# Performance work log

Hardware: AMD Instinct MI355X
Metric: run time of the kernel (lower is better)

## Reference

```python
import jax, jax.numpy as jnp
import numpy as np

E = 50000      # entity_total
R = 100        # relation_total
DIM = 128      # config.dim
M = 10         # max_context_num
M1 = M + 1
T = 2 * R + 2  # entity_gcn_weight rows (2R+1) + appended zero row
B = 1024


def setup_inputs() -> dict:
    key = jax.random.key(0)
    ks = jax.random.split(key, 40)
    f = jnp.float32
    stdv = 1.0 / np.sqrt(DIM)
    inp = {}
    inp['entity_emb'] = jax.random.normal(ks[0], (E, DIM), f) * 0.05
    inp['relation_emb'] = jax.random.normal(ks[1], (R, DIM), f) * 0.05
    ec = jax.random.normal(ks[2], (E + 1, DIM), f) * 0.05
    inp['entity_context'] = ec.at[E].set(0.0)   # padding_idx row = 0
    rc = jax.random.normal(ks[3], (R + 1, DIM), f) * 0.05
    inp['relation_context'] = rc.at[R].set(0.0)
    inp['entity_gcn_weight'] = jax.random.uniform(ks[4], (2 * R + 1, DIM, DIM), f, -stdv, stdv)
    inp['relation_gcn_weight'] = jax.random.uniform(ks[5], (DIM, DIM), f, -stdv, stdv)
    inp['gate_entity'] = jax.random.uniform(ks[6], (DIM,), f)
    inp['gate_relation'] = jax.random.uniform(ks[7], (DIM,), f)
    inp['v_ent'] = jax.random.uniform(ks[8], (DIM,), f)
    inp['v_rel'] = jax.random.uniform(ks[9], (DIM,), f)
    inp['pos_h'] = jax.random.randint(ks[10], (B,), 0, E)
    inp['pos_r'] = jax.random.randint(ks[11], (B,), 0, R)
    inp['pos_t'] = jax.random.randint(ks[12], (B,), 0, E)
    inp['neg_h'] = jax.random.randint(ks[13], (B,), 0, E)
    inp['neg_r'] = jax.random.randint(ks[14], (B,), 0, R)
    inp['neg_t'] = jax.random.randint(ks[15], (B,), 0, E)
    inp['ph_adj'] = jax.random.randint(ks[16], (B, M), 0, E + 1)
    inp['pt_adj'] = jax.random.randint(ks[17], (B, M), 0, E + 1)
    inp['nh_adj'] = jax.random.randint(ks[18], (B, M), 0, E + 1)
    inp['nt_adj'] = jax.random.randint(ks[19], (B, M), 0, E + 1)
    inp['pr_adj'] = jax.random.randint(ks[20], (B, M, 2), 0, R + 1)
    inp['nr_adj'] = jax.random.randint(ks[21], (B, M, 2), 0, R + 1)
    inp['ph_R'] = jax.random.randint(ks[22], (B, M1, M1), 0, T)
    inp['pt_R'] = jax.random.randint(ks[23], (B, M1, M1), 0, T)
    inp['nh_R'] = jax.random.randint(ks[24], (B, M1, M1), 0, T)
    inp['nt_R'] = jax.random.randint(ks[25], (B, M1, M1), 0, T)
    inp['ph_nn'] = jax.random.randint(ks[26], (B,), 0, M)
    inp['pt_nn'] = jax.random.randint(ks[27], (B,), 0, M)
    inp['nh_nn'] = jax.random.randint(ks[28], (B,), 0, M)
    inp['nt_nn'] = jax.random.randint(ks[29], (B,), 0, M)
    inp['ph_D'] = jax.random.uniform(ks[30], (B, M1, M1), f)
    inp['pt_D'] = jax.random.uniform(ks[31], (B, M1, M1), f)
    inp['nh_D'] = jax.random.uniform(ks[32], (B, M1, M1), f)
    inp['nt_D'] = jax.random.uniform(ks[33], (B, M1, M1), f)
    inp['pr_A'] = jax.random.normal(ks[34], (B, M1, M1), f)
    inp['nr_A'] = jax.random.normal(ks[35], (B, M1, M1), f)
    return inp


def reference(entity_emb, relation_emb, entity_context, relation_context,
              entity_gcn_weight, relation_gcn_weight, gate_entity, gate_relation,
              v_ent, v_rel,
              pos_h, pos_r, pos_t, neg_h, neg_r, neg_t,
              ph_adj, pt_adj, nh_adj, nt_adj, pr_adj, nr_adj,
              ph_R, pt_R, nh_R, nt_R, ph_nn, pt_nn, nh_nn, nt_nn,
              ph_D, pt_D, nh_D, nt_D, pr_A, nr_A):
    # weight table with trailing zero row (padding relation type T-1)
    Wfull = jnp.concatenate(
        [entity_gcn_weight, jnp.zeros((1, DIM, DIM), entity_gcn_weight.dtype)], axis=0)

    def ent_ctx(vec, adj_idx):
        # center vector + M gathered context vectors -> [B, M1, d]
        return jnp.concatenate([vec[:, None, :], entity_context[adj_idx]], axis=1)

    def rel_ctx(vec, adj_idx):
        # relation context comes in (head,tail) pairs, summed over the 2
        a = relation_context[adj_idx].sum(axis=2)  # [B, M, d]
        return jnp.concatenate([vec[:, None, :], a], axis=1)

    def rgcn(Rt, Dm, nn_, H):
        # vectorized R-GCN: out[b,j] = relu(sum_k D[b,j,k] * H[b,j] @ W[Rt[b,j,k]])
        # restricted to the dynamic (n+1)x(n+1) block via masking.
        j = jnp.arange(M1)
        valid = j[None, :] <= nn_[:, None]                 # [B, M1]
        pair = valid[:, :, None] & valid[:, None, :]       # [B, M1, M1]
        Rm = jnp.where(pair, Rt, T - 1)                    # pad -> zero weight
        Dd = jnp.where(pair, Dm, jnp.zeros((), Dm.dtype))
        # segment-reduce D over relation types: C[b,j,t] = sum_{k: Rm=t} D[b,j,k]
        C = (jax.nn.one_hot(Rm, T, dtype=H.dtype) * Dd[..., None]).sum(axis=2)  # [B,M1,T]
        S = jnp.einsum('bjt,tde->bjde', C, Wfull)          # [B, M1, d, d]
        out = jax.nn.relu(jnp.einsum('bjd,bjde->bje', H, S))
        return jnp.where(valid[..., None], out, jnp.zeros((), out.dtype))

    def gcn_rel(A, H):
        return jax.nn.relu(jnp.einsum('bij,bjd,de->bie', A, H, relation_gcn_weight))

    def subgraph(o, adj, v):
        # attention over context rows, then weighted sum
        tmp = jax.nn.relu(adj * o[:, None, :])             # [B, M1, d]
        alpha = jax.nn.softmax(tmp @ v, axis=1)            # [B, M1]
        return jnp.sum(alpha[..., None] * adj, axis=1)     # [B, d]

    p_h = entity_emb[pos_h]; p_t = entity_emb[pos_t]; p_r = relation_emb[pos_r]
    n_h = entity_emb[neg_h]; n_t = entity_emb[neg_t]; n_r = relation_emb[neg_r]

    ph_v = rgcn(ph_R, ph_D, ph_nn, ent_ctx(p_h, ph_adj))
    pt_v = rgcn(pt_R, pt_D, pt_nn, ent_ctx(p_t, pt_adj))
    nh_v = rgcn(nh_R, nh_D, nh_nn, ent_ctx(n_h, nh_adj))
    nt_v = rgcn(nt_R, nt_D, nt_nn, ent_ctx(n_t, nt_adj))
    pr_v = gcn_rel(pr_A, rel_ctx(p_r, pr_adj))
    nr_v = gcn_rel(nr_A, rel_ctx(n_r, nr_adj))

    ph_sg = subgraph(p_h, ph_v, v_ent); pt_sg = subgraph(p_t, pt_v, v_ent)
    nh_sg = subgraph(n_h, nh_v, v_ent); nt_sg = subgraph(n_t, nt_v, v_ent)
    pr_sg = subgraph(p_r, pr_v, v_rel); nr_sg = subgraph(n_r, nr_v, v_rel)

    ge = jax.nn.sigmoid(gate_entity)
    gr = jax.nn.sigmoid(gate_relation)
    ph_o = ge * p_h + (1 - ge) * ph_sg
    pt_o = ge * p_t + (1 - ge) * pt_sg
    nh_o = ge * n_h + (1 - ge) * nh_sg
    nt_o = ge * n_t + (1 - ge) * nt_sg
    pr_o = gr * p_r + (1 - gr) * pr_sg
    nr_o = gr * n_r + (1 - gr) * nr_sg

    p_score = jnp.linalg.norm(ph_o + pr_o - pt_o, ord=2, axis=1)
    n_score = jnp.linalg.norm(nh_o + nr_o - nt_o, ord=2, axis=1)
    return (p_score, n_score)
```

## Files before the change

### kernel.cpp

```cpp
#include <hip/hip_runtime.h>
#include <math.h>

#define B_   1024
#define M_   10
#define M1_  11
#define DIM_ 128
#define NW_  201
#define NQUAD_ (4*B_*M1_*M1_)
#define IPB_  64
#define SLOTS_ 2048
#define SCATB_ 121
#define WTILES_ ((NW_+1)*16)
#define HROWS_ (4*B_*M1_)
#define HROWB_ (HROWS_/16)
#define GEMMB_ (NW_*32)

typedef __attribute__((ext_vector_type(8))) short bf16x8;
typedef __attribute__((ext_vector_type(4))) float f32x4;

struct GatherPtrs {
    const int* center[4];
    const int* adj[4];
    const int* nn[4];
    const int* Rt[4];
    const float* Dm[4];
};

struct RelPtrs {
    const int* center[2];
    const int* adj2[2];
    const float* A[2];
};

__device__ __forceinline__ unsigned short f2bf(float f) {
    union { float f; unsigned u; } v; v.f = f;
    const unsigned r = v.u + 0x7FFFu + ((v.u >> 16) & 1u);
    return (unsigned short)(r >> 16);
}

template <int N>
__device__ __forceinline__ void block_reduce_bcast(float (&p)[N], float (*sred)[N],
                                                   int e, float (&sc)[N])
{
    #pragma unroll
    for (int off = 32; off; off >>= 1)
        #pragma unroll
        for (int i = 0; i < N; ++i) p[i] += __shfl_xor(p[i], off, 64);
    __syncthreads();
    if ((e & 63) == 0) {
        #pragma unroll
        for (int i = 0; i < N; ++i) sred[e >> 6][i] = p[i];
    }
    __syncthreads();
    #pragma unroll
    for (int i = 0; i < N; ++i) sc[i] = sred[0][i] + sred[1][i];
}

__device__ __forceinline__ float attn_pool(const float (&vm)[M1_], float o, float ve,
                                           float (*sred)[M1_], int e)
{
    float p[M1_];
    #pragma unroll
    for (int j = 0; j < M1_; ++j) p[j] = fmaxf(vm[j] * o, 0.f) * ve;
    float sc[M1_];
    block_reduce_bcast<M1_>(p, sred, e, sc);
    float mx = sc[0];
    #pragma unroll
    for (int j = 1; j < M1_; ++j) mx = fmaxf(mx, sc[j]);
    float s = 0.f, ex[M1_];
    #pragma unroll
    for (int j = 0; j < M1_; ++j) { ex[j] = expf(sc[j] - mx); s += ex[j]; }
    const float inv = 1.f / s;
    float sg = 0.f;
    #pragma unroll
    for (int j = 0; j < M1_; ++j) sg += ex[j] * inv * vm[j];
    return sg;
}

__global__ __launch_bounds__(256)
void prep_kernel(GatherPtrs gp,
                 const float* __restrict__ W, const float* __restrict__ Wr,
                 const float* __restrict__ ent_emb,
                 const float* __restrict__ ent_ctx,
                 unsigned short* __restrict__ WT,
                 unsigned short* __restrict__ Hd,
                 int* __restrict__ cursor, int* __restrict__ items)
{
    __shared__ int lh[NW_];
    __shared__ int lbase[NW_];
    __shared__ float tile[32][33];
    const int tid = threadIdx.x;
    const int bid = blockIdx.x;

    if (bid < SCATB_) {
        if (tid < NW_) lh[tid] = 0;
        __syncthreads();
        int rr[16], rk[16], pk[16];
        #pragma unroll
        for (int s = 0; s < 16; ++s) {
            const int idx = bid * 4096 + s * 256 + tid;
            const int c = idx / (B_ * M1_ * M1_);
            const int rem = idx % (B_ * M1_ * M1_);
            const int b = rem / (M1_ * M1_);
            const int jk = rem % (M1_ * M1_);
            const int j = jk / M1_, k = jk % M1_;
            const int n = gp.nn[c][b];
            rr[s] = -1;
            if (j <= n && k <= n) {
                const int r = gp.Rt[c][rem];
                if (r < NW_) {
                    rr[s] = r;
                    rk[s] = atomicAdd(&lh[r], 1);
                    pk[s] = (c << 18) | (b << 8) | (j << 4) | k;
                }
            }
        }
        __syncthreads();
        if (tid < NW_) lbase[tid] = lh[tid] ? atomicAdd(&cursor[tid], lh[tid]) : 0;
        __syncthreads();
        #pragma unroll
        for (int s = 0; s < 16; ++s)
            if (rr[s] >= 0) {
                const int slot = lbase[rr[s]] + rk[s];
                if (slot < SLOTS_) items[rr[s] * SLOTS_ + slot] = pk[s];
            }
    } else if (bid < SCATB_ + WTILES_) {
        const int tl = bid - SCATB_;
        const int t = tl >> 4, sub = tl & 15;
        const int bd = (sub >> 2) * 32, be = (sub & 3) * 32;
        const float* Ws = (t < NW_) ? (W + (size_t)t * DIM_ * DIM_) : Wr;
        unsigned short* Wd = WT + (size_t)t * DIM_ * DIM_;
        const int tx = tid & 31, ty = tid >> 5;
        #pragma unroll
        for (int r = 0; r < 32; r += 8)
            tile[r + ty][tx] = Ws[(bd + r + ty) * DIM_ + be + tx];
        __syncthreads();
        #pragma unroll
        for (int r = 0; r < 32; r += 8)
            Wd[(be + r + ty) * DIM_ + bd + tx] = f2bf(tile[tx][r + ty]);
    } else {
        const int rid = (bid - SCATB_ - WTILES_) * 16 + (tid >> 4);
        const int part = tid & 15;
        const int c = rid / (B_ * M1_);
        const int rem = rid % (B_ * M1_);
        const int b = rem / M1_, j = rem % M1_;
        const float* srow = (j == 0)
            ? ent_emb + (size_t)gp.center[c][b] * DIM_
            : ent_ctx + (size_t)gp.adj[c][b * M_ + (j - 1)] * DIM_;
        const float4* s4 = (const float4*)srow + part * 2;
        const float4 v0 = s4[0], v1 = s4[1];
        uint4 pkd;
        pkd.x = (unsigned)f2bf(v0.x) | ((unsigned)f2bf(v0.y) << 16);
        pkd.y = (unsigned)f2bf(v0.z) | ((unsigned)f2bf(v0.w) << 16);
        pkd.z = (unsigned)f2bf(v1.x) | ((unsigned)f2bf(v1.y) << 16);
        pkd.w = (unsigned)f2bf(v1.z) | ((unsigned)f2bf(v1.w) << 16);
        *reinterpret_cast<uint4*>(Hd + (size_t)rid * DIM_ + part * 8) = pkd;
    }
}

template <int MODE>
__global__ __launch_bounds__(256)
void rgcn_gemm(GatherPtrs gp,
               const float* __restrict__ ent_emb,
               const float* __restrict__ ent_ctx,
               const unsigned short* __restrict__ WT,
               const unsigned short* __restrict__ Hd,
               const int* __restrict__ items,
               const int* __restrict__ cursor,
               _Float16* __restrict__ partial,
               float* __restrict__ vent)
{
    __shared__ unsigned short sH[IPB_ * DIM_];
    __shared__ int sQ[IPB_];
    __shared__ float sD[IPB_];

    const int bid = blockIdx.x;
    const int t = bid >> 5, ch = bid & 31;
    const int cnt = min(cursor[t], SLOTS_);
    if (ch * IPB_ >= cnt) return;
    const int istart = ch * IPB_;
    const int nItems = min(IPB_, cnt - istart);
    const int tid = threadIdx.x;
    const int* ibase = items + t * SLOTS_;

    #pragma unroll
    for (int it4 = 0; it4 < 4; ++it4) {
        const int m = it4 * 256 + tid;
        const int it = m >> 4, chd = m & 15;
        uint4 pkd;
        if (it < nItems) {
            const int p = ibase[istart + it];
            const int c = p >> 18, b = (p >> 8) & 1023, j = (p >> 4) & 15, k = p & 15;
            const int row = (c * B_ + b) * M1_ + j;
            if (chd == 0) {
                sQ[it] = row * M1_ + k;
                sD[it] = gp.Dm[c][(b * M1_ + j) * M1_ + k];
            }
            if (MODE == 1) {
                pkd = *reinterpret_cast<const uint4*>(Hd + (size_t)row * DIM_ + chd * 8);
            } else {
                const float* srow = (j == 0)
                    ? ent_emb + (size_t)gp.center[c][b] * DIM_
                    : ent_ctx + (size_t)gp.adj[c][b * M_ + (j - 1)] * DIM_;
                const float4* s4 = (const float4*)srow + chd * 2;
                const float4 v0 = s4[0], v1 = s4[1];
                pkd.x = (unsigned)f2bf(v0.x) | ((unsigned)f2bf(v0.y) << 16);
                pkd.y = (unsigned)f2bf(v0.z) | ((unsigned)f2bf(v0.w) << 16);
                pkd.z = (unsigned)f2bf(v1.x) | ((unsigned)f2bf(v1.y) << 16);
                pkd.w = (unsigned)f2bf(v1.z) | ((unsigned)f2bf(v1.w) << 16);
            }
        } else {
            if (chd == 0) { sQ[it] = -1; sD[it] = 0.f; }
            pkd.x = pkd.y = pkd.z = pkd.w = 0u;
        }
        const int so = it * 256 + ((chd * 16) ^ ((it & 7) << 4));
        *reinterpret_cast<uint4*>(reinterpret_cast<char*>(sH) + so) = pkd;
    }
    __syncthreads();

    const int w = tid >> 6, l = tid & 63;
    const int lr = l & 15, lk = l >> 4;
    const unsigned short* Wp = WT + (size_t)t * DIM_ * DIM_;
    const f32x4 z = {0.f, 0.f, 0.f, 0.f};
    f32x4 acc[4][2];
    #pragma unroll
    for (int mi = 0; mi < 4; ++mi) { acc[mi][0] = z; acc[mi][1] = z; }

    #pragma unroll
    for (int kb = 0; kb < 4; ++kb) {
        const int o = kb * 64 + lk * 16;
        bf16x8 af[4], bfr[2];
        #pragma unroll
        for (int ni = 0; ni < 2; ++ni) {
            const int row = (2 * w + ni) * 16 + lr;
            bfr[ni] = *reinterpret_cast<const bf16x8*>(Wp + (size_t)row * DIM_ + kb * 32 + lk * 8);
        }
        #pragma unroll
        for (int mi = 0; mi < 4; ++mi) {
            const int row = mi * 16 + lr;
            af[mi] = *reinterpret_cast<const bf16x8*>(
                reinterpret_cast<const char*>(sH) + row * 256 + (o ^ ((row & 7) << 4)));
        }
        #pragma unroll
        for (int mi = 0; mi < 4; ++mi)
            #pragma unroll
            for (int ni = 0; ni < 2; ++ni)
                acc[mi][ni] = __builtin_amdgcn_mfma_f32_16x16x32_bf16(
                    af[mi], bfr[ni], acc[mi][ni], 0, 0, 0);
    }

    #pragma unroll
    for (int mi = 0; mi < 4; ++mi) {
        #pragma unroll
        for (int jj = 0; jj < 4; ++jj) {
            const int it = mi * 16 + lk * 4 + jj;
            const int q = sQ[it];
            if (q >= 0) {
                const float d = sD[it];
                #pragma unroll
                for (int ni = 0; ni < 2; ++ni) {
                    const int col = (2 * w + ni) * 16 + lr;
                    const float val = acc[mi][ni][jj] * d;
                    if (MODE <= 1) {
                        partial[(size_t)q * DIM_ + col] = (_Float16)val;
                    } else {
                        unsafeAtomicAdd(vent + (size_t)(q / M1_) * DIM_ + col, val);
                    }
                }
            }
        }
    }
}

template <bool FAST>
__global__ __launch_bounds__(128)
void pool_kernel(GatherPtrs gp, RelPtrs rp,
                 const float* __restrict__ ent_emb,
                 const float* __restrict__ rel_emb,
                 const float* __restrict__ rel_ctx,
                 const unsigned short* __restrict__ WT,
                 const float* __restrict__ v_ent,
                 const float* __restrict__ v_rel,
                 const _Float16* __restrict__ partial,
                 const float* __restrict__ vent,
                 float* __restrict__ sgbuf)
{
    __shared__ float sred[2][M1_];
    const int b = blockIdx.x, c = blockIdx.y, e = threadIdx.x;

    if (c < 4) {
        __shared__ int sRt[M1_ * M1_];
        const int n = gp.nn[c][b];
        if (FAST && e < M1_ * M1_) sRt[e] = gp.Rt[c][b * (M1_ * M1_) + e];
        __syncthreads();

        const float o = ent_emb[(size_t)gp.center[c][b] * DIM_ + e];
        float vm[M1_];
        if (FAST) {
            #pragma unroll
            for (int j = 0; j < M1_; ++j) {
                float s = 0.f;
                if (j <= n) {
                    const int base = (c * B_ + b) * (M1_ * M1_) + j * M1_;
                    #pragma unroll
                    for (int k = 0; k < M1_; ++k) {
                        const float v = (float)partial[(size_t)(base + k) * DIM_ + e];
                        s += (k <= n && sRt[j * M1_ + k] < NW_) ? v : 0.f;
                    }
                    s = fmaxf(s, 0.f);
                }
                vm[j] = s;
            }
        } else {
            const float* vmat = vent + ((size_t)(c * B_ + b)) * M1_ * DIM_;
            #pragma unroll
            for (int j = 0; j < M1_; ++j)
                vm[j] = (j <= n) ? fmaxf(vmat[j * DIM_ + e], 0.f) : 0.f;
        }
        const float sg = attn_pool(vm, o, v_ent[e], sred, e);
        sgbuf[((size_t)c * B_ + b) * DIM_ + e] = sg;
    } else {
        __shared__ float sA[M1_ * M1_];
        __shared__ unsigned short sAH[16 * DIM_];
        __shared__ float sOut[M1_][DIM_];
        const int cse = c - 4;
        const int* adj2 = rp.adj2[cse];

        float h[M1_];
        const float o = rel_emb[(size_t)rp.center[cse][b] * DIM_ + e];
        h[0] = o;
        #pragma unroll
        for (int j = 1; j < M1_; ++j) {
            const int a0 = adj2[((b * M_) + (j - 1)) * 2 + 0];
            const int a1 = adj2[((b * M_) + (j - 1)) * 2 + 1];
            h[j] = rel_ctx[(size_t)a0 * DIM_ + e] + rel_ctx[(size_t)a1 * DIM_ + e];
        }
        if (e < M1_ * M1_) sA[e] = rp.A[cse][b * (M1_ * M1_) + e];
        __syncthreads();

        #pragma unroll
        for (int i = 0; i < M1_; ++i) {
            float s = 0.f;
            #pragma unroll
            for (int jj = 0; jj < M1_; ++jj) s += sA[i * M1_ + jj] * h[jj];
            *reinterpret_cast<unsigned short*>(
                reinterpret_cast<char*>(sAH) + i * 256 + ((2 * e) ^ ((i & 7) << 4))) = f2bf(s);
        }
        #pragma unroll
        for (int i = M1_; i < 16; ++i)
            *reinterpret_cast<unsigned short*>(
                reinterpret_cast<char*>(sAH) + i * 256 + ((2 * e) ^ ((i & 7) << 4))) = 0;
        __syncthreads();

        const int w = e >> 6, l = e & 63;
        const int lr = l & 15, lk = l >> 4;
        const unsigned short* WrT = WT + (size_t)NW_ * DIM_ * DIM_;
        const f32x4 z = {0.f, 0.f, 0.f, 0.f};
        f32x4 acc[4] = {z, z, z, z};
        #pragma unroll
        for (int kb = 0; kb < 4; ++kb) {
            const bf16x8 af = *reinterpret_cast<const bf16x8*>(
                reinterpret_cast<const char*>(sAH) + lr * 256 + ((kb * 64 + lk * 16) ^ ((lr & 7) << 4)));
            #pragma unroll
            for (int ni = 0; ni < 4; ++ni) {
                const int cb = w * 4 + ni;
                const bf16x8 bfr = *reinterpret_cast<const bf16x8*>(
                    WrT + (size_t)(cb * 16 + lr) * DIM_ + kb * 32 + lk * 8);
                acc[ni] = __builtin_amdgcn_mfma_f32_16x16x32_bf16(af, bfr, acc[ni], 0, 0, 0);
            }
        }
        #pragma unroll
        for (int ni = 0; ni < 4; ++ni) {
            const int col = (w * 4 + ni) * 16 + lr;
            #pragma unroll
            for (int jj = 0; jj < 4; ++jj) {
                const int i = lk * 4 + jj;
                if (i < M1_) sOut[i][col] = fmaxf(acc[ni][jj], 0.f);
            }
        }
        __syncthreads();

        float vm[M1_];
        #pragma unroll
        for (int i = 0; i < M1_; ++i) vm[i] = sOut[i][e];
        const float sg = attn_pool(vm, o, v_rel[e], sred, e);
        sgbuf[((size_t)c * B_ + b) * DIM_ + e] = sg;
    }
}

__global__ __launch_bounds__(128)
void score_kernel(GatherPtrs gp,
                  const float* __restrict__ ent_emb,
                  const float* __restrict__ rel_emb,
                  const int* __restrict__ pos_r, const int* __restrict__ neg_r,
                  const float* __restrict__ gate_e, const float* __restrict__ gate_r,
                  const float* __restrict__ sgbuf,
                  float* __restrict__ out)
{
    __shared__ float sred[2][2];
    const int b = blockIdx.x, e = threadIdx.x;

    float cvec[4], osg[4];
    #pragma unroll
    for (int c = 0; c < 4; ++c) {
        cvec[c] = ent_emb[(size_t)gp.center[c][b] * DIM_ + e];
        osg[c] = sgbuf[((size_t)c * B_ + b) * DIM_ + e];
    }
    const float rvec0 = rel_emb[(size_t)pos_r[b] * DIM_ + e];
    const float rvec1 = rel_emb[(size_t)neg_r[b] * DIM_ + e];
    const float rsg0 = sgbuf[((size_t)4 * B_ + b) * DIM_ + e];
    const float rsg1 = sgbuf[((size_t)5 * B_ + b) * DIM_ + e];

    const float ge = 1.f / (1.f + expf(-gate_e[e]));
    const float gr = 1.f / (1.f + expf(-gate_r[e]));
    const float ph_o = ge * cvec[0] + (1.f - ge) * osg[0];
    const float pt_o = ge * cvec[1] + (1.f - ge) * osg[1];
    const float nh_o = ge * cvec[2] + (1.f - ge) * osg[2];
    const float nt_o = ge * cvec[3] + (1.f - ge) * osg[3];
    const float pr_o = gr * rvec0 + (1.f - gr) * rsg0;
    const float nr_o = gr * rvec1 + (1.f - gr) * rsg1;

    const float pv = ph_o + pr_o - pt_o;
    const float nv = nh_o + nr_o - nt_o;
    float p2[2] = { pv * pv, nv * nv };
    float sc2[2];
    block_reduce_bcast<2>(p2, sred, e, sc2);
    if (e == 0) { out[b] = sqrtf(sc2[0]); out[B_ + b] = sqrtf(sc2[1]); }
}

extern "C" void kernel_launch(void* const* d_in, const int* in_sizes, int n_in,
                              void* d_out, int out_size, void* d_ws, size_t ws_size,
                              hipStream_t stream)
{
    const float* entity_emb   = (const float*)d_in[0];
    const float* relation_emb = (const float*)d_in[1];
    const float* entity_ctx   = (const float*)d_in[2];
    const float* relation_ctx = (const float*)d_in[3];
    const float* egw          = (const float*)d_in[4];
    const float* rgw          = (const float*)d_in[5];
    const float* gate_e       = (const float*)d_in[6];
    const float* gate_r       = (const float*)d_in[7];
    const float* v_ent        = (const float*)d_in[8];
    const float* v_rel        = (const float*)d_in[9];
    const int* pos_h = (const int*)d_in[10];
    const int* pos_r = (const int*)d_in[11];
    const int* pos_t = (const int*)d_in[12];
    const int* neg_h = (const int*)d_in[13];
    const int* neg_r = (const int*)d_in[14];
    const int* neg_t = (const int*)d_in[15];
    const int* ph_adj = (const int*)d_in[16];
    const int* pt_adj = (const int*)d_in[17];
    const int* nh_adj = (const int*)d_in[18];
    const int* nt_adj = (const int*)d_in[19];
    const int* pr_adj = (const int*)d_in[20];
    const int* nr_adj = (const int*)d_in[21];
    const int* ph_R = (const int*)d_in[22];
    const int* pt_R = (const int*)d_in[23];
    const int* nh_R = (const int*)d_in[24];
    const int* nt_R = (const int*)d_in[25];
    const int* ph_nn = (const int*)d_in[26];
    const int* pt_nn = (const int*)d_in[27];
    const int* nh_nn = (const int*)d_in[28];
    const int* nt_nn = (const int*)d_in[29];
    const float* ph_D = (const float*)d_in[30];
    const float* pt_D = (const float*)d_in[31];
    const float* nh_D = (const float*)d_in[32];
    const float* nt_D = (const float*)d_in[33];
    const float* pr_A = (const float*)d_in[34];
    const float* nr_A = (const float*)d_in[35];

    GatherPtrs gp;
    gp.center[0] = pos_h; gp.center[1] = pos_t; gp.center[2] = neg_h; gp.center[3] = neg_t;
    gp.adj[0] = ph_adj; gp.adj[1] = pt_adj; gp.adj[2] = nh_adj; gp.adj[3] = nt_adj;
    gp.nn[0] = ph_nn; gp.nn[1] = pt_nn; gp.nn[2] = nh_nn; gp.nn[3] = nt_nn;
    gp.Rt[0] = ph_R; gp.Rt[1] = pt_R; gp.Rt[2] = nh_R; gp.Rt[3] = nt_R;
    gp.Dm[0] = ph_D; gp.Dm[1] = pt_D; gp.Dm[2] = nh_D; gp.Dm[3] = nt_D;

    RelPtrs rp;
    rp.center[0] = pos_r; rp.center[1] = neg_r;
    rp.adj2[0] = pr_adj; rp.adj2[1] = nr_adj;
    rp.A[0] = pr_A; rp.A[1] = nr_A;

    char* wsb = (char*)d_ws;
    const size_t partialBytes = (size_t)NQUAD_ * DIM_ * 2;
    const size_t itemsBytes   = (size_t)NW_ * SLOTS_ * 4;
    const size_t metaBytes    = 4096;
    const size_t wtBytes      = (size_t)(NW_ + 1) * DIM_ * DIM_ * 2;
    const size_t hdBytes      = (size_t)HROWS_ * DIM_ * 2;
    const size_t sgBytes      = (size_t)6 * B_ * DIM_ * 4;
    const size_t needB = partialBytes + itemsBytes + metaBytes + wtBytes;
    const size_t needA = needB + hdBytes;
    const int tier = (ws_size >= needA) ? 0 : (ws_size >= needB) ? 1 : 2;

    if (tier <= 1) {
        _Float16* partial = (_Float16*)wsb;
        int* items  = (int*)(wsb + partialBytes);
        int* cursor = (int*)(wsb + partialBytes + itemsBytes);
        char* wsg = wsb + partialBytes + itemsBytes + metaBytes;
        unsigned short* WT = (unsigned short*)wsg;
        float* sgbuf       = (float*)wsg;
        unsigned short* Hd = (tier == 0) ? (unsigned short*)(wsg + wtBytes) : nullptr;

        hipMemsetAsync(cursor, 0, 1024, stream);
        const int prepb = SCATB_ + WTILES_ + ((tier == 0) ? HROWB_ : 0);
        prep_kernel<<<dim3(prepb), dim3(256), 0, stream>>>(
            gp, egw, rgw, entity_emb, entity_ctx, WT, Hd, cursor, items);
        if (tier == 0) {
            rgcn_gemm<1><<<dim3(GEMMB_), dim3(256), 0, stream>>>(
                gp, entity_emb, entity_ctx, WT, Hd, items, cursor, partial, nullptr);
        } else {
            rgcn_gemm<0><<<dim3(GEMMB_), dim3(256), 0, stream>>>(
                gp, entity_emb, entity_ctx, WT, nullptr, items, cursor, partial, nullptr);
        }
        pool_kernel<true><<<dim3(B_, 6), dim3(128), 0, stream>>>(
            gp, rp, entity_emb, relation_emb, relation_ctx, WT,
            v_ent, v_rel, partial, nullptr, sgbuf);
        score_kernel<<<dim3(B_), dim3(128), 0, stream>>>(
            gp, entity_emb, relation_emb, pos_r, neg_r, gate_e, gate_r, sgbuf, (float*)d_out);
    } else {
        float* vent = (float*)wsb;
        const size_t ventBytes = (size_t)4 * B_ * M1_ * DIM_ * 4;
        unsigned short* WT = (unsigned short*)(wsb + ventBytes);
        float* sgbuf = (float*)(wsb + ventBytes + wtBytes);
        int* items   = (int*)(wsb + ventBytes + wtBytes + sgBytes);
        int* cursor  = (int*)(wsb + ventBytes + wtBytes + sgBytes + itemsBytes);

        hipMemsetAsync(vent, 0, ventBytes, stream);
        hipMemsetAsync(cursor, 0, 1024, stream);
        prep_kernel<<<dim3(SCATB_ + WTILES_), dim3(256), 0, stream>>>(
            gp, egw, rgw, entity_emb, entity_ctx, WT, nullptr, cursor, items);
        rgcn_gemm<2><<<dim3(GEMMB_), dim3(256), 0, stream>>>(
            gp, entity_emb, entity_ctx, WT, nullptr, items, cursor, nullptr, vent);
        pool_kernel<false><<<dim3(B_, 6), dim3(128), 0, stream>>>(
            gp, rp, entity_emb, relation_emb, relation_ctx, WT,
            v_ent, v_rel, nullptr, vent, sgbuf);
        score_kernel<<<dim3(B_), dim3(128), 0, stream>>>(
            gp, entity_emb, relation_emb, pos_r, neg_r, gate_e, gate_r, sgbuf, (float*)d_out);
    }
}
```

Before: 119.1 us.

## Drop bf16 H staging, precompute item rows and compact GEMM chunk list

Removes the bf16 pre-converted H row buffer and its prep blocks. The scatter phase now stores the resolved entity row index, the quad index and the D value for each item, so the GEMM gathers fp32 rows directly without decoding packed fields or doing indirect lookups. A new single-block kernel builds a compact table of non-empty (weight, chunk) pairs so GEMM blocks no longer launch only to exit early. In exchange it adds an extra kernel launch, larger item records, and direct fp32 gathers inside the GEMM.

```diff
diff --git a/kernel.cpp b/kernel.cpp
--- a/kernel.cpp
+++ b/kernel.cpp
@@ -9,11 +9,9 @@
 #define NQUAD_ (4*B_*M1_*M1_)
 #define IPB_  64
 #define SLOTS_ 2048
-#define SCATB_ 121
+#define SCATB_ 242
 #define WTILES_ ((NW_+1)*16)
-#define HROWS_ (4*B_*M1_)
-#define HROWB_ (HROWS_/16)
-#define GEMMB_ (NW_*32)
+#define MAXCHK_ (NW_ + NQUAD_/IPB_)
 
 typedef __attribute__((ext_vector_type(8))) short bf16x8;
 typedef __attribute__((ext_vector_type(4))) float f32x4;
@@ -80,11 +78,9 @@
 __global__ __launch_bounds__(256)
 void prep_kernel(GatherPtrs gp,
                  const float* __restrict__ W, const float* __restrict__ Wr,
-                 const float* __restrict__ ent_emb,
-                 const float* __restrict__ ent_ctx,
                  unsigned short* __restrict__ WT,
-                 unsigned short* __restrict__ Hd,
-                 int* __restrict__ cursor, int* __restrict__ items)
+                 int* __restrict__ cursor,
+                 int2* __restrict__ itemsEQ, float* __restrict__ itemsD)
 {
     __shared__ int lh[NW_];
     __shared__ int lbase[NW_];
@@ -95,10 +91,11 @@
     if (bid < SCATB_) {
         if (tid < NW_) lh[tid] = 0;
         __syncthreads();
-        int rr[16], rk[16], pk[16];
-        #pragma unroll
-        for (int s = 0; s < 16; ++s) {
-            const int idx = bid * 4096 + s * 256 + tid;
+        int rr[8], rk[8], ei[8], qv[8];
+        float dv[8];
+        #pragma unroll
+        for (int s = 0; s < 8; ++s) {
+            const int idx = bid * 2048 + s * 256 + tid;
             const int c = idx / (B_ * M1_ * M1_);
             const int rem = idx % (B_ * M1_ * M1_);
             const int b = rem / (M1_ * M1_);
@@ -111,7 +108,11 @@
                 if (r < NW_) {
                     rr[s] = r;
                     rk[s] = atomicAdd(&lh[r], 1);
-                    pk[s] = (c << 18) | (b << 8) | (j << 4) | k;
+                    const int eidx = (j == 0) ? gp.center[c][b]
+                                              : gp.adj[c][b * M_ + (j - 1)];
+                    ei[s] = (eidx << 1) | (j != 0);
+                    qv[s] = idx;
+                    dv[s] = gp.Dm[c][rem];
                 }
             }
         }
@@ -119,12 +120,15 @@
         if (tid < NW_) lbase[tid] = lh[tid] ? atomicAdd(&cursor[tid], lh[tid]) : 0;
         __syncthreads();
         #pragma unroll
-        for (int s = 0; s < 16; ++s)
+        for (int s = 0; s < 8; ++s)
             if (rr[s] >= 0) {
                 const int slot = lbase[rr[s]] + rk[s];
-                if (slot < SLOTS_) items[rr[s] * SLOTS_ + slot] = pk[s];
-            }
-    } else if (bid < SCATB_ + WTILES_) {
+                if (slot < SLOTS_) {
+                    itemsEQ[rr[s] * SLOTS_ + slot] = make_int2(ei[s], qv[s]);
+                    itemsD[rr[s] * SLOTS_ + slot] = dv[s];
+                }
+            }
+    } else {
         const int tl = bid - SCATB_;
         const int t = tl >> 4, sub = tl & 15;
         const int bd = (sub >> 2) * 32, be = (sub & 3) * 32;
@@ -138,35 +142,42 @@
         #pragma unroll
         for (int r = 0; r < 32; r += 8)
             Wd[(be + r + ty) * DIM_ + bd + tx] = f2bf(tile[tx][r + ty]);
-    } else {
-        const int rid = (bid - SCATB_ - WTILES_) * 16 + (tid >> 4);
-        const int part = tid & 15;
-        const int c = rid / (B_ * M1_);
-        const int rem = rid % (B_ * M1_);
-        const int b = rem / M1_, j = rem % M1_;
-        const float* srow = (j == 0)
-            ? ent_emb + (size_t)gp.center[c][b] * DIM_
-            : ent_ctx + (size_t)gp.adj[c][b * M_ + (j - 1)] * DIM_;
-        const float4* s4 = (const float4*)srow + part * 2;
-        const float4 v0 = s4[0], v1 = s4[1];
-        uint4 pkd;
-        pkd.x = (unsigned)f2bf(v0.x) | ((unsigned)f2bf(v0.y) << 16);
-        pkd.y = (unsigned)f2bf(v0.z) | ((unsigned)f2bf(v0.w) << 16);
-        pkd.z = (unsigned)f2bf(v1.x) | ((unsigned)f2bf(v1.y) << 16);
-        pkd.w = (unsigned)f2bf(v1.z) | ((unsigned)f2bf(v1.w) << 16);
-        *reinterpret_cast<uint4*>(Hd + (size_t)rid * DIM_ + part * 8) = pkd;
-    }
-}
-
-template <int MODE>
+    }
+}
+
 __global__ __launch_bounds__(256)
-void rgcn_gemm(GatherPtrs gp,
-               const float* __restrict__ ent_emb,
+void chunkbuild_kernel(const int* __restrict__ cursor,
+                       int* __restrict__ chunkTab, int* __restrict__ nchunks)
+{
+    __shared__ int nch[NW_];
+    __shared__ int bs[NW_ + 1];
+    const int t = threadIdx.x;
+    if (t < NW_) {
+        const int cnt = min(cursor[t], SLOTS_);
+        nch[t] = (cnt + IPB_ - 1) >> 6;
+    }
+    __syncthreads();
+    if (t == 0) {
+        int acc = 0;
+        for (int i = 0; i < NW_; ++i) { bs[i] = acc; acc += nch[i]; }
+        bs[NW_] = acc;
+        nchunks[0] = acc;
+    }
+    __syncthreads();
+    if (t < NW_)
+        for (int c = 0; c < nch[t]; ++c) chunkTab[bs[t] + c] = (t << 16) | c;
+}
+
+template <bool FAST>
+__global__ __launch_bounds__(256)
+void rgcn_gemm(const float* __restrict__ ent_emb,
                const float* __restrict__ ent_ctx,
                const unsigned short* __restrict__ WT,
-               const unsigned short* __restrict__ Hd,
-               const int* __restrict__ items,
+               const int2* __restrict__ itemsEQ,
+               const float* __restrict__ itemsD,
                const int* __restrict__ cursor,
+               const int* __restrict__ chunkTab,
+               const int* __restrict__ nchunks,
                _Float16* __restrict__ partial,
                float* __restrict__ vent)
 {
@@ -175,13 +186,14 @@
     __shared__ float sD[IPB_];
 
     const int bid = blockIdx.x;
-    const int t = bid >> 5, ch = bid & 31;
+    if (bid >= nchunks[0]) return;
+    const int ent = chunkTab[bid];
+    const int t = ent >> 16, ch = ent & 0xffff;
     const int cnt = min(cursor[t], SLOTS_);
-    if (ch * IPB_ >= cnt) return;
     const int istart = ch * IPB_;
     const int nItems = min(IPB_, cnt - istart);
     const int tid = threadIdx.x;
-    const int* ibase = items + t * SLOTS_;
+    const int2* eqBase = itemsEQ + t * SLOTS_ + istart;
 
     #pragma unroll
     for (int it4 = 0; it4 < 4; ++it4) {
@@ -189,26 +201,20 @@
         const int it = m >> 4, chd = m & 15;
         uint4 pkd;
         if (it < nItems) {
-            const int p = ibase[istart + it];
-            const int c = p >> 18, b = (p >> 8) & 1023, j = (p >> 4) & 15, k = p & 15;
-            const int row = (c * B_ + b) * M1_ + j;
+            const int2 eq = eqBase[it];
             if (chd == 0) {
-                sQ[it] = row * M1_ + k;
-                sD[it] = gp.Dm[c][(b * M1_ + j) * M1_ + k];
-            }
-            if (MODE == 1) {
-                pkd = *reinterpret_cast<const uint4*>(Hd + (size_t)row * DIM_ + chd * 8);
-            } else {
-                const float* srow = (j == 0)
-                    ? ent_emb + (size_t)gp.center[c][b] * DIM_
-                    : ent_ctx + (size_t)gp.adj[c][b * M_ + (j - 1)] * DIM_;
-                const float4* s4 = (const float4*)srow + chd * 2;
-                const float4 v0 = s4[0], v1 = s4[1];
-                pkd.x = (unsigned)f2bf(v0.x) | ((unsigned)f2bf(v0.y) << 16);
-                pkd.y = (unsigned)f2bf(v0.z) | ((unsigned)f2bf(v0.w) << 16);
-                pkd.z = (unsigned)f2bf(v1.x) | ((unsigned)f2bf(v1.y) << 16);
-                pkd.w = (unsigned)f2bf(v1.z) | ((unsigned)f2bf(v1.w) << 16);
-            }
+                sQ[it] = eq.y;
+                sD[it] = itemsD[t * SLOTS_ + istart + it];
+            }
+            const float* srow = (eq.x & 1)
+                ? ent_ctx + (size_t)(eq.x >> 1) * DIM_
+                : ent_emb + (size_t)(eq.x >> 1) * DIM_;
+            const float4* s4 = (const float4*)srow + chd * 2;
+            const float4 v0 = s4[0], v1 = s4[1];
+            pkd.x = (unsigned)f2bf(v0.x) | ((unsigned)f2bf(v0.y) << 16);
+            pkd.y = (unsigned)f2bf(v0.z) | ((unsigned)f2bf(v0.w) << 16);
+            pkd.z = (unsigned)f2bf(v1.x) | ((unsigned)f2bf(v1.y) << 16);
+            pkd.w = (unsigned)f2bf(v1.z) | ((unsigned)f2bf(v1.w) << 16);
         } else {
             if (chd == 0) { sQ[it] = -1; sD[it] = 0.f; }
             pkd.x = pkd.y = pkd.z = pkd.w = 0u;
@@ -261,7 +267,7 @@
                 for (int ni = 0; ni < 2; ++ni) {
                     const int col = (2 * w + ni) * 16 + lr;
                     const float val = acc[mi][ni][jj] * d;
-                    if (MODE <= 1) {
+                    if (FAST) {
                         partial[(size_t)q * DIM_ + col] = (_Float16)val;
                     } else {
                         unsafeAtomicAdd(vent + (size_t)(q / M1_) * DIM_ + col, val);
@@ -483,35 +489,33 @@
 
     char* wsb = (char*)d_ws;
     const size_t partialBytes = (size_t)NQUAD_ * DIM_ * 2;
-    const size_t itemsBytes   = (size_t)NW_ * SLOTS_ * 4;
-    const size_t metaBytes    = 4096;
+    const size_t eqBytes      = (size_t)NW_ * SLOTS_ * 8;
+    const size_t dBytes       = (size_t)NW_ * SLOTS_ * 4;
+    const size_t metaBytes    = 65536;
     const size_t wtBytes      = (size_t)(NW_ + 1) * DIM_ * DIM_ * 2;
-    const size_t hdBytes      = (size_t)HROWS_ * DIM_ * 2;
     const size_t sgBytes      = (size_t)6 * B_ * DIM_ * 4;
-    const size_t needB = partialBytes + itemsBytes + metaBytes + wtBytes;
-    const size_t needA = needB + hdBytes;
-    const int tier = (ws_size >= needA) ? 0 : (ws_size >= needB) ? 1 : 2;
-
-    if (tier <= 1) {
+    const size_t fastNeed = partialBytes + eqBytes + dBytes + metaBytes + wtBytes;
+    const bool fast = (ws_size >= fastNeed);
+
+    if (fast) {
         _Float16* partial = (_Float16*)wsb;
-        int* items  = (int*)(wsb + partialBytes);
-        int* cursor = (int*)(wsb + partialBytes + itemsBytes);
-        char* wsg = wsb + partialBytes + itemsBytes + metaBytes;
+        int2* itemsEQ = (int2*)(wsb + partialBytes);
+        float* itemsD = (float*)(wsb + partialBytes + eqBytes);
+        char* meta    = wsb + partialBytes + eqBytes + dBytes;
+        int* cursor   = (int*)meta;
+        int* nchunks  = (int*)(meta + 1024);
+        int* chunkTab = (int*)(meta + 2048);
+        char* wsg = wsb + partialBytes + eqBytes + dBytes + metaBytes;
         unsigned short* WT = (unsigned short*)wsg;
         float* sgbuf       = (float*)wsg;
-        unsigned short* Hd = (tier == 0) ? (unsigned short*)(wsg + wtBytes) : nullptr;
 
         hipMemsetAsync(cursor, 0, 1024, stream);
-        const int prepb = SCATB_ + WTILES_ + ((tier == 0) ? HROWB_ : 0);
-        prep_kernel<<<dim3(prepb), dim3(256), 0, stream>>>(
-            gp, egw, rgw, entity_emb, entity_ctx, WT, Hd, cursor, items);
-        if (tier == 0) {
-            rgcn_gemm<1><<<dim3(GEMMB_), dim3(256), 0, stream>>>(
-                gp, entity_emb, entity_ctx, WT, Hd, items, cursor, partial, nullptr);
-        } else {
-            rgcn_gemm<0><<<dim3(GEMMB_), dim3(256), 0, stream>>>(
-                gp, entity_emb, entity_ctx, WT, nullptr, items, cursor, partial, nullptr);
-        }
+        prep_kernel<<<dim3(SCATB_ + WTILES_), dim3(256), 0, stream>>>(
+            gp, egw, rgw, WT, cursor, itemsEQ, itemsD);
+        chunkbuild_kernel<<<dim3(1), dim3(256), 0, stream>>>(cursor, chunkTab, nchunks);
+        rgcn_gemm<true><<<dim3(MAXCHK_), dim3(256), 0, stream>>>(
+            entity_emb, entity_ctx, WT, itemsEQ, itemsD, cursor, chunkTab, nchunks,
+            partial, nullptr);
         pool_kernel<true><<<dim3(B_, 6), dim3(128), 0, stream>>>(
             gp, rp, entity_emb, relation_emb, relation_ctx, WT,
             v_ent, v_rel, partial, nullptr, sgbuf);
@@ -521,16 +525,22 @@
         float* vent = (float*)wsb;
         const size_t ventBytes = (size_t)4 * B_ * M1_ * DIM_ * 4;
         unsigned short* WT = (unsigned short*)(wsb + ventBytes);
-        float* sgbuf = (float*)(wsb + ventBytes + wtBytes);
-        int* items   = (int*)(wsb + ventBytes + wtBytes + sgBytes);
-        int* cursor  = (int*)(wsb + ventBytes + wtBytes + sgBytes + itemsBytes);
+        float* sgbuf  = (float*)(wsb + ventBytes + wtBytes);
+        int2* itemsEQ = (int2*)(wsb + ventBytes + wtBytes + sgBytes);
+        float* itemsD = (float*)(wsb + ventBytes + wtBytes + sgBytes + eqBytes);
+        char* meta    = wsb + ventBytes + wtBytes + sgBytes + eqBytes + dBytes;
+        int* cursor   = (int*)meta;
+        int* nchunks  = (int*)(meta + 1024);
+        int* chunkTab = (int*)(meta + 2048);
 
         hipMemsetAsync(vent, 0, ventBytes, stream);
         hipMemsetAsync(cursor, 0, 1024, stream);
         prep_kernel<<<dim3(SCATB_ + WTILES_), dim3(256), 0, stream>>>(
-            gp, egw, rgw, entity_emb, entity_ctx, WT, nullptr, cursor, items);
-        rgcn_gemm<2><<<dim3(GEMMB_), dim3(256), 0, stream>>>(
-            gp, entity_emb, entity_ctx, WT, nullptr, items, cursor, nullptr, vent);
+            gp, egw, rgw, WT, cursor, itemsEQ, itemsD);
+        chunkbuild_kernel<<<dim3(1), dim3(256), 0, stream>>>(cursor, chunkTab, nchunks);
+        rgcn_gemm<false><<<dim3(MAXCHK_), dim3(256), 0, stream>>>(
+            entity_emb, entity_ctx, WT, itemsEQ, itemsD, cursor, chunkTab, nchunks,
+            nullptr, vent);
         pool_kernel<false><<<dim3(B_, 6), dim3(128), 0, stream>>>(
             gp, rp, entity_emb, relation_emb, relation_ctx, WT,
             v_ent, v_rel, nullptr, vent, sgbuf);
```

Measured after the change: 95.78 us, median of 2. 19.6% less time.
